# Kernel optimization log

Hardware: AMD Instinct MI355X
Metric: run time of the kernel (lower is better)

## Reference

```python
import jax, jax.numpy as jnp
import numpy as np

B, N, C = 8, 89, 1024
H = C // 2  # adaptor hidden dim = channel_in // 2


def _mlp2(t, W1, b1, W2, b2):
    # MLP(channel_in, [channel_in, channel_out]): Linear -> ReLU -> Linear
    return jax.nn.relu(t @ W1 + b1) @ W2 + b2


def setup_inputs() -> dict:
    key = jax.random.key(0)
    ks = jax.random.split(key, 12)
    g = lambda k, shape, fan: jax.random.normal(k, shape, jnp.float32) * (fan ** -0.5)
    return {
        "x": jax.random.normal(ks[0], (B, N, C), jnp.float32),
        # two independently learned dense adjacencies (AddConv / ModulatorConv)
        "adj_add": jax.random.normal(ks[1], (N, N), jnp.float32),
        "adj_mod": jax.random.normal(ks[2], (N, N), jnp.float32),
        # Adaptor MLP: C -> C -> H -> 1
        "Wa1": g(ks[3], (C, C), C), "ba1": jnp.zeros((C,), jnp.float32),
        "Wa2": g(ks[4], (C, H), C), "ba2": jnp.zeros((H,), jnp.float32),
        "Wa3": g(ks[5], (H, 1), H), "ba3": jnp.zeros((1,), jnp.float32),
        # mlp_add: C -> C -> C
        "Wadd1": g(ks[6], (C, C), C), "badd1": jnp.zeros((C,), jnp.float32),
        "Wadd2": g(ks[7], (C, C), C), "badd2": jnp.zeros((C,), jnp.float32),
        # mlp_mod: C -> C -> C
        "Wmod1": g(ks[8], (C, C), C), "bmod1": jnp.zeros((C,), jnp.float32),
        "Wmod2": g(ks[9], (C, C), C), "bmod2": jnp.zeros((C,), jnp.float32),
    }


def reference(x, adj_add, adj_mod, Wa1, ba1, Wa2, ba2, Wa3, ba3,
              Wadd1, badd1, Wadd2, badd2, Wmod1, bmod1, Wmod2, bmod2):
    # dense_to_sparse on an all-nonzero learned randn adj => fully connected graph;
    # PyG convention: edge_index[0]=row=source j, edge_index[1]=col=target i,
    # so aggregation at node i sums over adj[j, i] * message(j -> i).

    # Adaptor: per-edge gate s_{b,j,i} = sigmoid(MLP(x_j * x_i))
    p = x[:, :, None, :] * x[:, None, :, :]              # [B, Nsrc, Ndst, C]
    h = jax.nn.relu(p @ Wa1 + ba1)                       # [B, N, N, C]
    h = jax.nn.relu(h @ Wa2 + ba2)                       # [B, N, N, H]
    s = jax.nn.sigmoid((h @ Wa3 + ba3)[..., 0])          # [B, Nsrc, Ndst]

    # AddConv: out[b,i,f] = sum_j s[b,j,i] * adj_add[j,i] * x[b,j,f]
    a_t = jnp.einsum('bji,ji,bjf->bif', s, adj_add, x)
    # ModulatorConv: out[b,i,f] = x[b,i,f] * sum_j adj_mod[j,i] * x[b,j,f]
    m_t = x * jnp.einsum('ji,bjf->bif', adj_mod, x)

    out_add = _mlp2(a_t, Wadd1, badd1, Wadd2, badd2)
    out_mod = _mlp2(m_t, Wmod1, bmod1, Wmod2, bmod2)
    return (x + out_add + out_mod) / 3.0
```

## Files before the change

kernel.cpp:

```cpp
#include <hip/hip_runtime.h>

typedef unsigned short u16;
typedef unsigned int   u32;
typedef __attribute__((ext_vector_type(8))) short bf16x8;
typedef __attribute__((ext_vector_type(4))) float f32x4;

#define DEVFN __device__ __forceinline__

DEVFN float b2f(u16 u){ u32 t=((u32)u)<<16; float f; __builtin_memcpy(&f,&t,4); return f; }
DEVFN u16 f2b(float f){ u32 t; __builtin_memcpy(&t,&f,4); t += 0x7fffu + ((t>>16)&1u); return (u16)(t>>16); }

DEVFN void row2ji(int row, int* jj, int* ii){
  int j = (int)((179.0f - sqrtf(179.0f*179.0f - 8.0f*(float)row)) * 0.5f);
  if(j < 0) j = 0; if(j > 88) j = 88;
  while(j < 88 && (j+1)*(179-(j+1))/2 <= row) j++;
  while(j > 0 && j*(179-j)/2 > row) j--;
  *jj = j;
  *ii = j + (row - j*(179-j)/2);
}

struct TrArgs { const float* src; u16* dst; int C; };
struct TrPack { TrArgs a[6]; };

DEVFN void pgen_body(const float* __restrict__ x, u16* __restrict__ p, long pz,
                     int z, int b, int row, int tid){
  int j, i; row2ji(row < 4005 ? row : 0, &j, &i);
  const float* xb = x + (size_t)b*91136;
  int c = tid*4;
  float4 a  = *(const float4*)(xb + (size_t)j*1024 + c);
  float4 bb = *(const float4*)(xb + (size_t)i*1024 + c);
  ushort4 o;
  o.x = f2b(a.x*bb.x);
  o.y = f2b(a.y*bb.y);
  o.z = f2b(a.z*bb.z);
  o.w = f2b(a.w*bb.w);
  *(ushort4*)(p + (size_t)z*pz + (size_t)row*1024 + c) = o;
}

__global__ __launch_bounds__(256) void prep_k(TrPack pk, float* __restrict__ logit,
                                              const float* __restrict__ x,
                                              u16* __restrict__ pbuf, long pz){
  __shared__ u16 tile[32][33];
  int id = blockIdx.x, tid = threadIdx.x;
  if(id < 6144){
    TrArgs t = pk.a[id>>10];
    int q = id & 1023;
    int bx = (q&31)*32, by = (q>>5)*32;
    if(bx >= t.C) return;
    int tx = tid&31, ty = tid>>5;
    #pragma unroll
    for(int yy=ty; yy<32; yy+=8) tile[yy][tx] = f2b(t.src[(size_t)(by+yy)*t.C + bx+tx]);
    __syncthreads();
    #pragma unroll
    for(int yy=ty; yy<32; yy+=8) t.dst[(size_t)(bx+yy)*1024 + by+tx] = tile[tx][yy];
  } else if(id < 6176){
    int idx = (id-6144)*1024 + tid*4;
    *(float4*)(logit + idx) = (float4){0.f,0.f,0.f,0.f};
  } else {
    int pid = id - 6176;
    int z = pid >> 12, row = pid & 4095;
    pgen_body(x, pbuf, pz, z, z, row, tid);
  }
}

__global__ __launch_bounds__(256) void pgen_k(const float* __restrict__ x,
                                              u16* __restrict__ p, long pz, int bbase){
  pgen_body(x, p, pz, blockIdx.y, bbase + blockIdx.y, blockIdx.x, threadIdx.x);
}

DEVFN void stage_gl(const u16* __restrict__ g0, u16* lds0, int tid){
  int w = tid>>6, lane = tid&63;
  #pragma unroll
  for(int i=0;i<4;i++){
    int p  = (w*4+i)*64 + lane;
    int r  = p>>3;
    int kb = (p&7) ^ (r&7);
    const u16* g = g0 + ((size_t)r<<10) + (kb<<3);
    u16* l = lds0 + (size_t)(w*4+i)*512;
    __builtin_amdgcn_global_load_lds((const __attribute__((address_space(1))) u32*)g,
                                     (__attribute__((address_space(3))) u32*)l, 16, 0, 0);
  }
}

template<int AMODE, int EPI>
__global__ __launch_bounds__(256,2) void gemm_k(
    const u16* __restrict__ A0, const u16* __restrict__ B0,
    const u16* __restrict__ A1, const u16* __restrict__ B1,
    const float* __restrict__ bias0, const float* __restrict__ bias1,
    const float* __restrict__ aux,
    void* __restrict__ out,
    long a0z, long oz, int ldo, int aux2 , int kiters,
    int mmask, int mshift, int mlimit)
{
  int by = blockIdx.y;
  int m0 = (by & mmask)*128, n0 = (by >> mshift)*128, z = blockIdx.z;
  if(m0 >= mlimit) return;

  __shared__ __align__(16) u16 As[128*64];
  __shared__ __align__(16) u16 Bs[128*64];
  int tid = threadIdx.x;

  const u16* Abase0;
  const u16* Bbase0;
  if(AMODE==2){
    Abase0 = (z ? A1 : A0) + (size_t)m0*1024;
    Bbase0 = (z ? B1 : B0) + (size_t)n0*1024;
  } else {
    Abase0 = A0 + (size_t)z*a0z + (size_t)m0*1024;
    Bbase0 = B0 + (size_t)n0*1024;
  }

  f32x4 acc[4][4];
  #pragma unroll
  for(int a=0;a<4;a++)
    #pragma unroll
    for(int b=0;b<4;b++) acc[a][b] = (f32x4){0.f,0.f,0.f,0.f};

  int w = tid>>6, lane = tid&63, quad = lane>>4, l15 = lane&15;
  int wr = (w>>1)*64, wc = (w&1)*64;

  for(int kk=0; kk<kiters; kk++){
    int k0 = (kk & 15) << 6;
    const u16* Ab = Abase0 + k0;
    const u16* Bb = Bbase0 + k0;
    if(AMODE==1 && kk>=16){
      Ab = A1 + (size_t)m0*1024 + k0;
      Bb = B1 + (size_t)n0*1024 + k0;
    }
    __syncthreads();
    stage_gl(Ab, As, tid);
    stage_gl(Bb, Bs, tid);
    __syncthreads();
    #pragma unroll
    for(int kq=0; kq<2; kq++){
      int kbl = kq*4 + quad;
      bf16x8 af[4], bfv[4];
      #pragma unroll
      for(int t=0;t<4;t++){
        int rr = wr + t*16 + l15;
        af[t] = *(const bf16x8*)(As + rr*64 + ((kbl ^ (rr&7))<<3));
      }
      #pragma unroll
      for(int t=0;t<4;t++){
        int cc = wc + t*16 + l15;
        bfv[t] = *(const bf16x8*)(Bs + cc*64 + ((kbl ^ (cc&7))<<3));
      }
      #pragma unroll
      for(int rt=0;rt<4;rt++)
        #pragma unroll
        for(int ct=0;ct<4;ct++)
          acc[rt][ct] = __builtin_amdgcn_mfma_f32_16x16x32_bf16(af[rt], bfv[ct], acc[rt][ct], 0,0,0);
    }
  }

  float bc[4], w3[4];
  const float* bsel = (AMODE==2 && z) ? bias1 : bias0;
  #pragma unroll
  for(int ct=0;ct<4;ct++){
    int colg = n0 + wc + ct*16 + l15;
    bc[ct] = bsel[colg];
    if(EPI==1) bc[ct] += bias1[colg];
    if(EPI==2) w3[ct] = aux[colg];
  }

  if(EPI==2){
    float part[4][4];
    #pragma unroll
    for(int rt=0;rt<4;rt++)
      #pragma unroll
      for(int r=0;r<4;r++) part[rt][r] = 0.f;
    #pragma unroll
    for(int rt=0;rt<4;rt++)
      #pragma unroll
      for(int ct=0;ct<4;ct++)
        #pragma unroll
        for(int r=0;r<4;r++)
          part[rt][r] += fmaxf(acc[rt][ct][r] + bc[ct], 0.f) * w3[ct];
    #pragma unroll
    for(int m=1;m<16;m<<=1)
      #pragma unroll
      for(int rt=0;rt<4;rt++)
        #pragma unroll
        for(int r=0;r<4;r++)
          part[rt][r] += __shfl_xor(part[rt][r], m, 64);
    if(l15==0){
      float* lo = (float*)out + (size_t)(aux2 + z)*4096;
      #pragma unroll
      for(int rt=0;rt<4;rt++)
        #pragma unroll
        for(int r=0;r<4;r++)
          atomicAdd(lo + (m0 + wr + rt*16 + quad*4 + r), part[rt][r]);
    }
    return;
  }

  #pragma unroll
  for(int ct=0;ct<4;ct++){
    int colg = n0 + wc + ct*16 + l15;
    #pragma unroll
    for(int rt=0;rt<4;rt++){
      #pragma unroll
      for(int r=0;r<4;r++){
        int rowg = m0 + wr + rt*16 + quad*4 + r;
        float v = acc[rt][ct][r] + bc[ct];
        if(EPI==0){
          v = fmaxf(v, 0.f);
          ((u16*)out)[(size_t)z*oz + (size_t)rowg*ldo + colg] = f2b(v);
        } else {
          if(rowg < aux2){
            v = (v + aux[(size_t)rowg*1024 + colg]) * (1.f/3.f);
            ((float*)out)[(size_t)rowg*ldo + colg] = v;
          }
        }
      }
    }
  }
}

__global__ __launch_bounds__(256) void k4_k(const float* __restrict__ x,
    const float* __restrict__ adjA, const float* __restrict__ adjM,
    const float* __restrict__ logit, const float* __restrict__ ba3,
    u16* __restrict__ a_t, u16* __restrict__ m_t)
{
  int b = blockIdx.y, i = blockIdx.x, t = threadIdx.x;
  __shared__ float ca[89], cm[89];
  if(t < 89){
    int tri = (t<=i) ? t*(179-t)/2 + (i-t) : i*(179-i)/2 + (t-i);
    float lg = logit[(size_t)b*4096 + tri] + ba3[0];
    float sv = 1.f/(1.f + expf(-lg));
    ca[t] = sv * adjA[t*89 + i];
    cm[t] = adjM[t*89 + i];
  }
  __syncthreads();
  const float* xb = x + (size_t)b*91136;
  int c0 = t*4;
  float aa0=0,aa1=0,aa2=0,aa3=0, am0=0,am1=0,am2=0,am3=0;
  for(int j=0;j<89;j++){
    float4 xv = *(const float4*)(xb + (size_t)j*1024 + c0);
    float fa=ca[j], fm=cm[j];
    aa0+=fa*xv.x; aa1+=fa*xv.y; aa2+=fa*xv.z; aa3+=fa*xv.w;
    am0+=fm*xv.x; am1+=fm*xv.y; am2+=fm*xv.z; am3+=fm*xv.w;
  }
  float4 xi = *(const float4*)(xb + (size_t)i*1024 + c0);
  size_t ro = ((size_t)(b*89 + i))*1024 + c0;
  ushort4 oa; oa.x=f2b(aa0); oa.y=f2b(aa1); oa.z=f2b(aa2); oa.w=f2b(aa3);
  ushort4 om;
  om.x=f2b(xi.x*am0); om.y=f2b(xi.y*am1);
  om.z=f2b(xi.z*am2); om.w=f2b(xi.w*am3);
  *(ushort4*)(a_t + ro) = oa;
  *(ushort4*)(m_t + ro) = om;
}

extern "C" void kernel_launch(void* const* d_in, const int* in_sizes, int n_in,
                              void* d_out, int out_size, void* d_ws, size_t ws_size,
                              hipStream_t stream)
{
  const float* X     = (const float*)d_in[0];
  const float* adjA  = (const float*)d_in[1];
  const float* adjM  = (const float*)d_in[2];
  const float* Wa1   = (const float*)d_in[3];
  const float* ba1   = (const float*)d_in[4];
  const float* Wa2   = (const float*)d_in[5];
  const float* ba2   = (const float*)d_in[6];
  const float* Wa3   = (const float*)d_in[7];
  const float* ba3   = (const float*)d_in[8];
  const float* Wadd1 = (const float*)d_in[9];
  const float* badd1 = (const float*)d_in[10];
  const float* Wadd2 = (const float*)d_in[11];
  const float* badd2 = (const float*)d_in[12];
  const float* Wmod1 = (const float*)d_in[13];
  const float* bmod1 = (const float*)d_in[14];
  const float* Wmod2 = (const float*)d_in[15];
  const float* bmod2 = (const float*)d_in[16];

  char* w = (char*)d_ws;
  u16* WaT1   = (u16*)w; w += (size_t)1024*1024*2;
  u16* WaT2   = (u16*)w; w += (size_t)512*1024*2;
  u16* WaddT1 = (u16*)w; w += (size_t)1024*1024*2;
  u16* WaddT2 = (u16*)w; w += (size_t)1024*1024*2;
  u16* WmodT1 = (u16*)w; w += (size_t)1024*1024*2;
  u16* WmodT2 = (u16*)w; w += (size_t)1024*1024*2;
  float* logit= (float*)w; w += (size_t)8*4096*4;
  u16* a_t    = (u16*)w; w += (size_t)768*1024*2;
  u16* m_t    = (u16*)w; w += (size_t)768*1024*2;
  u16* ha     = (u16*)w; w += (size_t)768*1024*2;
  u16* hm     = (u16*)w; w += (size_t)768*1024*2;
  size_t fixed = (size_t)(w - (char*)d_ws);
  size_t per_p = (size_t)4096*1024*2, per_h1 = (size_t)4096*1024*2;
  bool flat = ws_size >= fixed + 8*(per_p + per_h1);
  int nb = flat ? 8 : 1;
  u16* pbuf = (u16*)w; w += per_p  * nb;
  u16* h1   = (u16*)w;

  TrPack tp;
  tp.a[0].src = Wa1;   tp.a[0].dst = WaT1;   tp.a[0].C = 1024;
  tp.a[1].src = Wa2;   tp.a[1].dst = WaT2;   tp.a[1].C = 512;
  tp.a[2].src = Wadd1; tp.a[2].dst = WaddT1; tp.a[2].C = 1024;
  tp.a[3].src = Wadd2; tp.a[3].dst = WaddT2; tp.a[3].C = 1024;
  tp.a[4].src = Wmod1; tp.a[4].dst = WmodT1; tp.a[4].C = 1024;
  tp.a[5].src = Wmod2; tp.a[5].dst = WmodT2; tp.a[5].C = 1024;

  long pz = 4096*1024, h1z = 4096*1024;
  prep_k<<<dim3(6176 + 4096*nb), 256, 0, stream>>>(tp, logit, X, pbuf, pz);

  for(int bb=0; bb<8; bb+=nb){
    if(bb) pgen_k<<<dim3(4096,nb),256,0,stream>>>(X, pbuf, pz, bb);
    gemm_k<0,0><<<dim3(1,256,nb),256,0,stream>>>(pbuf, WaT1, nullptr,nullptr, ba1,nullptr, nullptr,
                                                 h1, pz, h1z, 1024, 4096, 16, 31, 5, 4096);
    gemm_k<0,2><<<dim3(1,128,nb),256,0,stream>>>(h1, WaT2, nullptr,nullptr, ba2,nullptr, Wa3,
                                                 logit, h1z, 0, 0, bb, 16, 31, 5, 4096);
  }
  k4_k<<<dim3(89,8),256,0,stream>>>(X, adjA, adjM, logit, ba3, a_t, m_t);
  gemm_k<2,0><<<dim3(1,64,2),256,0,stream>>>(a_t, WaddT1, m_t, WmodT1, badd1, bmod1, nullptr,
                                             ha, 0, (long)768*1024, 1024, 768, 16, 7, 3, 768);
  gemm_k<1,1><<<dim3(1,64,1),256,0,stream>>>(ha, WaddT2, hm, WmodT2, badd2, bmod2, X,
                                             (float*)d_out, 0, 0, 1024, 712, 32, 7, 3, 768);
}
```

Measured before the change: 318.0 us.

## Use 64-row tiles and split-K atomics for the small output MLP GEMMs

Adds a templated M-tile size to the GEMM and uses 64-row tiles for the two small post-aggregation GEMMs, doubling their block count. The final GEMM stops concatenating K across the add and mod branches and instead runs each branch as a separate z-slice that atomically accumulates into a zeroed output, with the residual and biases added only by slice 0. The bf16 ReLU epilogue now stages the tile through LDS to issue 16-byte coalesced stores. The intent is to fill more CUs on the tail GEMMs, at the cost of an extra memset and fp32 atomics.

Result: faster. 299.0 us (-6.0%).

```diff
diff --git a/kernel.cpp b/kernel.cpp
--- a/kernel.cpp
+++ b/kernel.cpp
@@ -68,21 +68,23 @@
   pgen_body(x, p, pz, blockIdx.y, bbase + blockIdx.y, blockIdx.x, threadIdx.x);
 }
 
+template<int ROWS>
 DEVFN void stage_gl(const u16* __restrict__ g0, u16* lds0, int tid){
+  constexpr int IT = ROWS/32;
   int w = tid>>6, lane = tid&63;
   #pragma unroll
-  for(int i=0;i<4;i++){
-    int p  = (w*4+i)*64 + lane;
+  for(int i=0;i<IT;i++){
+    int p  = (w*IT+i)*64 + lane;
     int r  = p>>3;
     int kb = (p&7) ^ (r&7);
     const u16* g = g0 + ((size_t)r<<10) + (kb<<3);
-    u16* l = lds0 + (size_t)(w*4+i)*512;
+    u16* l = lds0 + (size_t)(w*IT+i)*512;
     __builtin_amdgcn_global_load_lds((const __attribute__((address_space(1))) u32*)g,
                                      (__attribute__((address_space(3))) u32*)l, 16, 0, 0);
   }
 }
 
-template<int AMODE, int EPI>
+template<int AMODE, int EPI, int TM>
 __global__ __launch_bounds__(256,2) void gemm_k(
     const u16* __restrict__ A0, const u16* __restrict__ B0,
     const u16* __restrict__ A1, const u16* __restrict__ B1,
@@ -92,12 +94,14 @@
     long a0z, long oz, int ldo, int aux2 , int kiters,
     int mmask, int mshift, int mlimit)
 {
+  constexpr int MB = TM/32;
   int by = blockIdx.y;
-  int m0 = (by & mmask)*128, n0 = (by >> mshift)*128, z = blockIdx.z;
+  int m0 = (by & mmask)*TM, n0 = (by >> mshift)*128, z = blockIdx.z;
   if(m0 >= mlimit) return;
 
-  __shared__ __align__(16) u16 As[128*64];
-  __shared__ __align__(16) u16 Bs[128*64];
+  __shared__ __align__(16) u16 smem[TM*64 + 128*64];
+  u16* As = smem;
+  u16* Bs = smem + TM*64;
   int tid = threadIdx.x;
 
   const u16* Abase0;
@@ -110,33 +114,29 @@
     Bbase0 = B0 + (size_t)n0*1024;
   }
 
-  f32x4 acc[4][4];
-  #pragma unroll
-  for(int a=0;a<4;a++)
+  f32x4 acc[MB][4];
+  #pragma unroll
+  for(int a=0;a<MB;a++)
     #pragma unroll
     for(int b=0;b<4;b++) acc[a][b] = (f32x4){0.f,0.f,0.f,0.f};
 
   int w = tid>>6, lane = tid&63, quad = lane>>4, l15 = lane&15;
-  int wr = (w>>1)*64, wc = (w&1)*64;
+  int wr = (w>>1)*(TM/2), wc = (w&1)*64;
 
   for(int kk=0; kk<kiters; kk++){
     int k0 = (kk & 15) << 6;
     const u16* Ab = Abase0 + k0;
     const u16* Bb = Bbase0 + k0;
-    if(AMODE==1 && kk>=16){
-      Ab = A1 + (size_t)m0*1024 + k0;
-      Bb = B1 + (size_t)n0*1024 + k0;
-    }
     __syncthreads();
-    stage_gl(Ab, As, tid);
-    stage_gl(Bb, Bs, tid);
+    stage_gl<TM >(Ab, As, tid);
+    stage_gl<128>(Bb, Bs, tid);
     __syncthreads();
     #pragma unroll
     for(int kq=0; kq<2; kq++){
       int kbl = kq*4 + quad;
-      bf16x8 af[4], bfv[4];
-      #pragma unroll
-      for(int t=0;t<4;t++){
+      bf16x8 af[MB], bfv[4];
+      #pragma unroll
+      for(int t=0;t<MB;t++){
         int rr = wr + t*16 + l15;
         af[t] = *(const bf16x8*)(As + rr*64 + ((kbl ^ (rr&7))<<3));
       }
@@ -146,7 +146,7 @@
         bfv[t] = *(const bf16x8*)(Bs + cc*64 + ((kbl ^ (cc&7))<<3));
       }
       #pragma unroll
-      for(int rt=0;rt<4;rt++)
+      for(int rt=0;rt<MB;rt++)
         #pragma unroll
         for(int ct=0;ct<4;ct++)
           acc[rt][ct] = __builtin_amdgcn_mfma_f32_16x16x32_bf16(af[rt], bfv[ct], acc[rt][ct], 0,0,0);
@@ -154,23 +154,25 @@
   }
 
   float bc[4], w3[4];
-  const float* bsel = (AMODE==2 && z) ? bias1 : bias0;
   #pragma unroll
   for(int ct=0;ct<4;ct++){
     int colg = n0 + wc + ct*16 + l15;
-    bc[ct] = bsel[colg];
-    if(EPI==1) bc[ct] += bias1[colg];
-    if(EPI==2) w3[ct] = aux[colg];
+    if(EPI==3){
+      bc[ct] = (z==0) ? (bias0[colg] + bias1[colg]) : 0.f;
+    } else {
+      bc[ct] = (AMODE==2 && z) ? bias1[colg] : bias0[colg];
+      if(EPI==2) w3[ct] = aux[colg];
+    }
   }
 
   if(EPI==2){
-    float part[4][4];
-    #pragma unroll
-    for(int rt=0;rt<4;rt++)
+    float part[MB][4];
+    #pragma unroll
+    for(int rt=0;rt<MB;rt++)
       #pragma unroll
       for(int r=0;r<4;r++) part[rt][r] = 0.f;
     #pragma unroll
-    for(int rt=0;rt<4;rt++)
+    for(int rt=0;rt<MB;rt++)
       #pragma unroll
       for(int ct=0;ct<4;ct++)
         #pragma unroll
@@ -179,14 +181,14 @@
     #pragma unroll
     for(int m=1;m<16;m<<=1)
       #pragma unroll
-      for(int rt=0;rt<4;rt++)
+      for(int rt=0;rt<MB;rt++)
         #pragma unroll
         for(int r=0;r<4;r++)
           part[rt][r] += __shfl_xor(part[rt][r], m, 64);
     if(l15==0){
       float* lo = (float*)out + (size_t)(aux2 + z)*4096;
       #pragma unroll
-      for(int rt=0;rt<4;rt++)
+      for(int rt=0;rt<MB;rt++)
         #pragma unroll
         for(int r=0;r<4;r++)
           atomicAdd(lo + (m0 + wr + rt*16 + quad*4 + r), part[rt][r]);
@@ -194,26 +196,49 @@
     return;
   }
 
-  #pragma unroll
-  for(int ct=0;ct<4;ct++){
-    int colg = n0 + wc + ct*16 + l15;
-    #pragma unroll
-    for(int rt=0;rt<4;rt++){
-      #pragma unroll
-      for(int r=0;r<4;r++){
-        int rowg = m0 + wr + rt*16 + quad*4 + r;
-        float v = acc[rt][ct][r] + bc[ct];
-        if(EPI==0){
-          v = fmaxf(v, 0.f);
-          ((u16*)out)[(size_t)z*oz + (size_t)rowg*ldo + colg] = f2b(v);
-        } else {
+  if(EPI==3){
+    const float third = 1.f/3.f;
+    float* op = (float*)out;
+    #pragma unroll
+    for(int ct=0;ct<4;ct++){
+      int colg = n0 + wc + ct*16 + l15;
+      #pragma unroll
+      for(int rt=0;rt<MB;rt++){
+        #pragma unroll
+        for(int r=0;r<4;r++){
+          int rowg = m0 + wr + rt*16 + quad*4 + r;
           if(rowg < aux2){
-            v = (v + aux[(size_t)rowg*1024 + colg]) * (1.f/3.f);
-            ((float*)out)[(size_t)rowg*ldo + colg] = v;
+            float v = acc[rt][ct][r];
+            if(z==0) v += aux[(size_t)rowg*1024 + colg] + bc[ct];
+            atomicAdd(op + (size_t)rowg*1024 + colg, v*third);
           }
         }
       }
     }
+    return;
+  }
+
+  __syncthreads();
+  u16* Ct = smem;
+  #pragma unroll
+  for(int ct=0;ct<4;ct++){
+    int cl = wc + ct*16 + l15;
+    #pragma unroll
+    for(int rt=0;rt<MB;rt++){
+      #pragma unroll
+      for(int r=0;r<4;r++){
+        int rl = wr + rt*16 + quad*4 + r;
+        Ct[rl*128 + cl] = f2b(fmaxf(acc[rt][ct][r] + bc[ct], 0.f));
+      }
+    }
+  }
+  __syncthreads();
+  u16* outp = (u16*)out + (size_t)z*oz;
+  #pragma unroll
+  for(int i=0;i<TM/16;i++){
+    int q = i*256 + tid;
+    int row = q>>4, c16 = q&15;
+    *(uint4*)(outp + (size_t)(m0+row)*ldo + n0 + c16*8) = *(const uint4*)(Ct + row*128 + c16*8);
   }
 }
 
@@ -305,14 +330,15 @@
 
   for(int bb=0; bb<8; bb+=nb){
     if(bb) pgen_k<<<dim3(4096,nb),256,0,stream>>>(X, pbuf, pz, bb);
-    gemm_k<0,0><<<dim3(1,256,nb),256,0,stream>>>(pbuf, WaT1, nullptr,nullptr, ba1,nullptr, nullptr,
-                                                 h1, pz, h1z, 1024, 4096, 16, 31, 5, 4096);
-    gemm_k<0,2><<<dim3(1,128,nb),256,0,stream>>>(h1, WaT2, nullptr,nullptr, ba2,nullptr, Wa3,
-                                                 logit, h1z, 0, 0, bb, 16, 31, 5, 4096);
+    gemm_k<0,0,128><<<dim3(1,256,nb),256,0,stream>>>(pbuf, WaT1, nullptr,nullptr, ba1,nullptr, nullptr,
+                                                     h1, pz, h1z, 1024, 4096, 16, 31, 5, 4096);
+    gemm_k<0,2,128><<<dim3(1,128,nb),256,0,stream>>>(h1, WaT2, nullptr,nullptr, ba2,nullptr, Wa3,
+                                                     logit, h1z, 0, 0, bb, 16, 31, 5, 4096);
   }
   k4_k<<<dim3(89,8),256,0,stream>>>(X, adjA, adjM, logit, ba3, a_t, m_t);
-  gemm_k<2,0><<<dim3(1,64,2),256,0,stream>>>(a_t, WaddT1, m_t, WmodT1, badd1, bmod1, nullptr,
-                                             ha, 0, (long)768*1024, 1024, 768, 16, 7, 3, 768);
-  gemm_k<1,1><<<dim3(1,64,1),256,0,stream>>>(ha, WaddT2, hm, WmodT2, badd2, bmod2, X,
-                                             (float*)d_out, 0, 0, 1024, 712, 32, 7, 3, 768);
-}
+  gemm_k<2,0,64><<<dim3(1,128,2),256,0,stream>>>(a_t, WaddT1, m_t, WmodT1, badd1, bmod1, nullptr,
+                                                 ha, 0, (long)768*1024, 1024, 768, 16, 15, 4, 768);
+  hipMemsetAsync(d_out, 0, (size_t)out_size*4, stream);
+  gemm_k<2,3,64><<<dim3(1,128,2),256,0,stream>>>(ha, WaddT2, hm, WmodT2, badd2, bmod2, X,
+                                                 d_out, 0, 0, 1024, 712, 16, 15, 4, 768);
+}
```
